# Optimization experiments

Measured on AMD Instinct MI355X. Metric: run time of the kernel, lower is better.

The kernel has to match this reference:

```python
import jax, jax.numpy as jnp
import numpy as np

N = 50000
E = 800000
IN_DIM = 128
HID = 64
OUT_DIM = 128
NEG_SLOPE = 0.2  # PyG GATConv default


def _add_self_loops(src, dst, edge_attr, n):
    # PyG GATConv(add_self_loops=True) with edge_dim uses fill_value='mean':
    # self-loop edge_attr = mean of edge_attr of incoming edges per node.
    deg = jax.ops.segment_sum(jnp.ones((src.shape[0],), edge_attr.dtype), dst, num_segments=n)
    loop_attr = jax.ops.segment_sum(edge_attr, dst, num_segments=n) / jnp.maximum(deg, 1.0)[:, None]
    loop = jnp.arange(n, dtype=src.dtype)
    return (jnp.concatenate([src, loop]), jnp.concatenate([dst, loop]),
            jnp.concatenate([edge_attr, loop_attr], axis=0))


def _gat_conv(x, src, dst, edge_attr, W, We, a_src, a_dst, a_edge, bias, heads, out_dim, concat, n):
    src, dst, edge_attr = _add_self_loops(src, dst, edge_attr, n)
    h = (x @ W).reshape(n, heads, out_dim)                      # [N,H,D]
    he = (edge_attr @ We).reshape(-1, heads, out_dim)           # [E',H,D]
    alpha_src = jnp.einsum('nhd,hd->nh', h, a_src)
    alpha_dst = jnp.einsum('nhd,hd->nh', h, a_dst)
    alpha_edge = jnp.einsum('ehd,hd->eh', he, a_edge)
    alpha = jax.nn.leaky_relu(alpha_src[src] + alpha_dst[dst] + alpha_edge, NEG_SLOPE)  # [E',H]
    # segment softmax over edges grouped by destination node
    amax = jax.ops.segment_max(alpha, dst, num_segments=n)
    amax = jnp.where(jnp.isfinite(amax), amax, 0.0)
    ex = jnp.exp(alpha - amax[dst])
    denom = jax.ops.segment_sum(ex, dst, num_segments=n)
    coef = ex / (denom[dst] + 1e-16)                            # [E',H]
    msg = h[src] * coef[:, :, None]                             # [E',H,D]
    out = jax.ops.segment_sum(msg, dst, num_segments=n)         # [N,H,D]
    out = out.reshape(n, heads * out_dim) if concat else out.mean(axis=1)
    return out + bias


def setup_inputs() -> dict:
    key = jax.random.key(0)
    ks = jax.random.split(key, 16)
    s = 0.05
    inp = {
        'x': jax.random.normal(ks[0], (N, IN_DIM), jnp.float32),
        'edge_index': jax.random.randint(ks[1], (2, E), 0, N, dtype=jnp.int64),
        'edge_attr': jax.random.normal(ks[2], (E, 2), jnp.float32),
        # gat1: heads=4, concat -> out 4*HID
        'W1': jax.random.normal(ks[3], (IN_DIM, 4 * HID), jnp.float32) * s,
        'We1': jax.random.normal(ks[4], (2, 4 * HID), jnp.float32) * s,
        'asrc1': jax.random.normal(ks[5], (4, HID), jnp.float32) * s,
        'adst1': jax.random.normal(ks[6], (4, HID), jnp.float32) * s,
        'aedge1': jax.random.normal(ks[7], (4, HID), jnp.float32) * s,
        'b1': jnp.zeros((4 * HID,), jnp.float32),
        # gat2: heads=1, concat=False -> out OUT_DIM
        'W2': jax.random.normal(ks[8], (4 * HID, OUT_DIM), jnp.float32) * s,
        'We2': jax.random.normal(ks[9], (2, OUT_DIM), jnp.float32) * s,
        'asrc2': jax.random.normal(ks[10], (1, OUT_DIM), jnp.float32) * s,
        'adst2': jax.random.normal(ks[11], (1, OUT_DIM), jnp.float32) * s,
        'aedge2': jax.random.normal(ks[12], (1, OUT_DIM), jnp.float32) * s,
        'b2': jnp.zeros((OUT_DIM,), jnp.float32),
    }
    return inp


def reference(x, edge_index, edge_attr, W1, We1, asrc1, adst1, aedge1, b1,
              W2, We2, asrc2, adst2, aedge2, b2):
    src, dst = edge_index[0], edge_index[1]
    # dropout layers are identity in eval mode
    h = _gat_conv(x, src, dst, edge_attr, W1, We1, asrc1, adst1, aedge1, b1,
                  heads=4, out_dim=HID, concat=True, n=x.shape[0])
    h = jax.nn.elu(h)
    out = _gat_conv(h, src, dst, edge_attr, W2, We2, asrc2, adst2, aedge2, b2,
                    heads=1, out_dim=OUT_DIM, concat=False, n=x.shape[0])
    return out
```

## Files before the change

### kernel.cpp

```cpp
#include <hip/hip_runtime.h>
#include <hip/hip_bf16.h>

#define NN 50000
#define EE 800000
#define EP (EE + NN)
#define SCAN_B 2048
#define NB ((NN + SCAN_B - 1) / SCAN_B)


typedef short bf16x8 __attribute__((ext_vector_type(8)));
typedef float f32x4  __attribute__((ext_vector_type(4)));

__device__ __forceinline__ float bf2f(unsigned short u) {
    return __uint_as_float(((unsigned)u) << 16);
}
__device__ __forceinline__ unsigned short f2bf(float f) {
    unsigned b = __float_as_uint(f);
    b += 0x7fffu + ((b >> 16) & 1u);
    return (unsigned short)(b >> 16);
}
__device__ __forceinline__ float2 bfpair(unsigned u) {
    return make_float2(__uint_as_float(u << 16), __uint_as_float(u & 0xffff0000u));
}

__global__ void k_prep(const float* __restrict__ We1, const float* __restrict__ ae1,
                       const float* __restrict__ We2, const float* __restrict__ ae2,
                       float* __restrict__ v,
                       const float* __restrict__ W1, unsigned short* __restrict__ W1t,
                       const float* __restrict__ W2, unsigned short* __restrict__ W2t,
                       const int* __restrict__ ei, int* __restrict__ idg,
                       const float* __restrict__ x, unsigned short* __restrict__ xb) {
    int bid = blockIdx.x, t = threadIdx.x;
    if (bid == 0) {
        if (t < 8) {
            int c = t >> 2, h = t & 3;
            float s = 0.f;
            for (int d = 0; d < 64; d++) s += We1[c * 256 + h * 64 + d] * ae1[h * 64 + d];
            v[c * 4 + h] = s;
        } else if (t < 10) {
            int c = t - 8;
            float s = 0.f;
            for (int d = 0; d < 128; d++) s += We2[c * 128 + d] * ae2[d];
            v[8 + c] = s;
        }
    } else if (bid <= 256) {
        int idx = (bid - 1) * 256 + t;
        if (idx < 32768) {
            int k = idx >> 8, n = idx & 255;
            W1t[n * 128 + k] = f2bf(W1[idx]);
        } else {
            int i = idx - 32768;
            int k = i >> 7, n = i & 127;
            W2t[n * 256 + k] = f2bf(W2[i]);
        }
    } else if (bid <= 256 + 3125) {
        int e = (bid - 257) * 256 + t;
        if (e < EE) atomicAdd(&idg[ei[EE + e]], 1);
    } else {
        int i = (bid - 3382) * 256 + t;
        if (i < NN * 128 / 4) {
            float4 vv = ((const float4*)x)[i];
            ushort4 o;
            o.x = f2bf(vv.x); o.y = f2bf(vv.y); o.z = f2bf(vv.z); o.w = f2bf(vv.w);
            ((ushort4*)xb)[i] = o;
        }
    }
}

__global__ void k_scan1(const int* __restrict__ idg, int* __restrict__ rowptr,
                        int* __restrict__ bsum) {
    __shared__ int sh[512];
    int t = threadIdx.x;
    int base = blockIdx.x * SCAN_B + t * 4;
    int v[4]; int s = 0;
    #pragma unroll
    for (int j = 0; j < 4; j++) {
        int i = base + j;
        v[j] = (i < NN) ? (idg[i] + 1) : 0;
        s += v[j];
    }
    sh[t] = s;
    __syncthreads();
    for (int off = 1; off < 512; off <<= 1) {
        int a = (t >= off) ? sh[t - off] : 0;
        __syncthreads();
        sh[t] += a;
        __syncthreads();
    }
    int run = sh[t] - s;
    #pragma unroll
    for (int j = 0; j < 4; j++) {
        int i = base + j;
        if (i < NN) rowptr[i] = run;
        run += v[j];
    }
    if (t == 511) bsum[blockIdx.x] = sh[511];
}

__global__ void k_scan2(const int* __restrict__ bsum, int* __restrict__ boff,
                        int* __restrict__ rowptr) {
    if (threadIdx.x == 0) {
        int acc = 0;
        for (int b = 0; b < NB; b++) { boff[b] = acc; acc += bsum[b]; }
        rowptr[NN] = acc;
    }
}

__global__ void k_scan3(int* __restrict__ rowptr, const int* __restrict__ boff) {
    int t = threadIdx.x;
    int i = blockIdx.x * SCAN_B + t * 4;
    int off = boff[blockIdx.x];
    #pragma unroll
    for (int j = 0; j < 4; j++)
        if (i + j < NN) rowptr[i + j] += off;
}

__global__ void k_scatter(const int* __restrict__ ei, const float* __restrict__ eattr,
                          const int* __restrict__ rowptr, int* __restrict__ cnt,
                          int2* __restrict__ slot) {
    int e = blockIdx.x * blockDim.x + threadIdx.x;
    if (e >= EE) return;
    int s = ei[e], d = ei[EE + e];
    int p = rowptr[d] + 1 + atomicAdd(&cnt[d], 1);
    float2 a = ((const float2*)eattr)[e];
    unsigned a0 = f2bf(a.x), a1 = f2bf(a.y);
    slot[p] = make_int2(s, (int)(a0 | (a1 << 16)));
}

__global__ void k_selfattr(const int* __restrict__ rowptr, int2* __restrict__ slot) {
    int n = blockIdx.x * blockDim.x + threadIdx.x;
    if (n >= NN) return;
    int beg = rowptr[n], end = rowptr[n + 1];
    float s0 = 0.f, s1 = 0.f;
    for (int p = beg + 1; p < end; p++) {
        unsigned a = (unsigned)slot[p].y;
        s0 += bf2f((unsigned short)(a & 0xffff));
        s1 += bf2f((unsigned short)(a >> 16));
    }
    float dg = fmaxf((float)(end - beg - 1), 1.0f);
    unsigned b0 = f2bf(s0 / dg), b1v = f2bf(s1 / dg);
    slot[beg] = make_int2(n, (int)(b0 | (b1v << 16)));
}

template <int K, int NT, int H>
__global__ __launch_bounds__(256) void gemm_mfma(const unsigned short* __restrict__ A,
                                                 const unsigned short* __restrict__ Bt,
                                                 unsigned short* __restrict__ C,
                                                 const float* __restrict__ avs,
                                                 const float* __restrict__ avd,
                                                 float* __restrict__ asrc,
                                                 float* __restrict__ adst,
                                                 int M, int N) {
    int wave = threadIdx.x >> 6, lane = threadIdx.x & 63;
    int l16 = lane & 15, quad = lane >> 4;
    int m0 = blockIdx.y * 128 + wave * 32;
    int n0 = blockIdx.x * (NT * 16);

    f32x4 acc[2][NT];
    #pragma unroll
    for (int mt = 0; mt < 2; mt++)
        #pragma unroll
        for (int nt = 0; nt < NT; nt++)
            acc[mt][nt] = (f32x4){0.f, 0.f, 0.f, 0.f};

    int ar0 = min(m0 + l16, M - 1);
    int ar1 = min(m0 + 16 + l16, M - 1);
    const unsigned short* a0 = A + (size_t)ar0 * K + quad * 8;
    const unsigned short* a1 = A + (size_t)ar1 * K + quad * 8;
    const unsigned short* bp = Bt + (size_t)(n0 + l16) * K + quad * 8;

    #pragma unroll
    for (int k0 = 0; k0 < K; k0 += 32) {
        bf16x8 af0 = *(const bf16x8*)(a0 + k0);
        bf16x8 af1 = *(const bf16x8*)(a1 + k0);
        #pragma unroll
        for (int nt = 0; nt < NT; nt++) {
            bf16x8 bf = *(const bf16x8*)(bp + (size_t)nt * 16 * K + k0);
            acc[0][nt] = __builtin_amdgcn_mfma_f32_16x16x32_bf16(af0, bf, acc[0][nt], 0, 0, 0);
            acc[1][nt] = __builtin_amdgcn_mfma_f32_16x16x32_bf16(af1, bf, acc[1][nt], 0, 0, 0);
        }
    }

    #pragma unroll
    for (int mt = 0; mt < 2; mt++)
        #pragma unroll
        for (int reg = 0; reg < 4; reg++) {
            int row = m0 + mt * 16 + quad * 4 + reg;
            if (row < M) {
                #pragma unroll
                for (int nt = 0; nt < NT; nt++)
                    C[(size_t)row * N + n0 + nt * 16 + l16] = f2bf(acc[mt][nt][reg]);
            }
        }

    float ws[NT], wd[NT];
    #pragma unroll
    for (int nt = 0; nt < NT; nt++) {
        ws[nt] = avs[n0 + nt * 16 + l16];
        wd[nt] = avd[n0 + nt * 16 + l16];
    }
    int hh = n0 >> 6;
    #pragma unroll
    for (int mt = 0; mt < 2; mt++)
        #pragma unroll
        for (int reg = 0; reg < 4; reg++) {
            int row = m0 + mt * 16 + quad * 4 + reg;
            float s1 = 0.f, s2 = 0.f;
            #pragma unroll
            for (int nt = 0; nt < NT; nt++) {
                float c = acc[mt][nt][reg];
                s1 += c * ws[nt];
                s2 += c * wd[nt];
            }
            #pragma unroll
            for (int off = 1; off < 16; off <<= 1) {
                s1 += __shfl_xor(s1, off);
                s2 += __shfl_xor(s2, off);
            }
            if (l16 == 0 && row < M) {
                asrc[row * H + hh] = s1;
                adst[row * H + hh] = s2;
            }
        }
}

__global__ __launch_bounds__(256) void k_agg1(const int* __restrict__ rowptr,
                       const int2* __restrict__ slot, const float* __restrict__ asrc,
                       const float* __restrict__ adst, const float* __restrict__ v,
                       const unsigned short* __restrict__ hb, const float* __restrict__ b1,
                       unsigned short* __restrict__ h2b) {
    int node = blockIdx.x * 4 + (threadIdx.x >> 6);
    if (node >= NN) return;
    int lane = threadIdx.x & 63;
    int j    = lane & 15;
    int hp   = lane >> 4;
    int half = lane >> 5;
    int hl   = lane & 31;
    int hh2  = hl >> 3;
    int beg = rowptr[node], end = rowptr[node + 1];
    float ad_p = adst[node * 4 + hp];
    float v0 = v[hp], v1 = v[4 + hp];
    float2 acc2[4] = {};
    float den = 0.f;
    for (int pb = beg; pb < end; pb += 16) {
        int m = min(16, end - pb);
        int sj = 0; float exv = 0.f;
        if (j < m) {
            int2 sl = slot[pb + j];
            sj = sl.x;
            float2 a = bfpair((unsigned)sl.y);
            float al = asrc[sj * 4 + hp] + ad_p + a.x * v0 + a.y * v1;
            al = (al > 0.f) ? al : 0.2f * al;
            exv = __expf(al);
        }
        den += exv;
        #pragma unroll 2
        for (int j2 = 0; j2 < m; j2 += 2) {
            int jj = j2 + half;
            int s   = __shfl(sj, jj);
            float w = __shfl(exv, jj + (hh2 << 4));
            uint4 raw = *(const uint4*)(hb + (size_t)s * 256 + hl * 8);
            float2 p0 = bfpair(raw.x), p1 = bfpair(raw.y);
            float2 p2 = bfpair(raw.z), p3 = bfpair(raw.w);
            acc2[0].x += w * p0.x; acc2[0].y += w * p0.y;
            acc2[1].x += w * p1.x; acc2[1].y += w * p1.y;
            acc2[2].x += w * p2.x; acc2[2].y += w * p2.y;
            acc2[3].x += w * p3.x; acc2[3].y += w * p3.y;
        }
    }
    #pragma unroll
    for (int k = 0; k < 4; k++) {
        acc2[k].x += __shfl_down(acc2[k].x, 32);
        acc2[k].y += __shfl_down(acc2[k].y, 32);
    }
    #pragma unroll
    for (int off = 8; off; off >>= 1) den += __shfl_xor(den, off);
    float den_h = __shfl(den, hh2 << 4);
    if (lane < 32) {
        float inv = 1.f / (den_h + 1e-16f);
        short ov[8];
        #pragma unroll
        for (int k = 0; k < 4; k++) {
            float va = acc2[k].x * inv + b1[hl * 8 + 2 * k];
            float vb = acc2[k].y * inv + b1[hl * 8 + 2 * k + 1];
            va = (va > 0.f) ? va : __expf(va) - 1.f;
            vb = (vb > 0.f) ? vb : __expf(vb) - 1.f;
            ov[2 * k]     = (short)f2bf(va);
            ov[2 * k + 1] = (short)f2bf(vb);
        }
        bf16x8 o = {ov[0], ov[1], ov[2], ov[3], ov[4], ov[5], ov[6], ov[7]};
        *(bf16x8*)(h2b + (size_t)node * 256 + hl * 8) = o;
    }
}

__global__ __launch_bounds__(256) void k_agg2(const int* __restrict__ rowptr,
                       const int2* __restrict__ slot, const float* __restrict__ asrc,
                       const float* __restrict__ adst, const float* __restrict__ v,
                       const unsigned short* __restrict__ gb, const float* __restrict__ b2,
                       float* __restrict__ outp) {
    int node = blockIdx.x * 4 + (threadIdx.x >> 6);
    if (node >= NN) return;
    int lane = threadIdx.x & 63;
    int q  = lane >> 4;
    int ql = lane & 15;
    int beg = rowptr[node], end = rowptr[node + 1];
    float ad = adst[node];
    float v0 = v[0], v1 = v[1];
    float2 acc2[4] = {};
    float den = 0.f;
    for (int pb = beg; pb < end; pb += 64) {
        int m = min(64, end - pb);
        int sj = 0; float exv = 0.f;
        if (lane < m) {
            int2 sl = slot[pb + lane];
            sj = sl.x;
            float2 a = bfpair((unsigned)sl.y);
            float al = asrc[sj] + ad + a.x * v0 + a.y * v1;
            al = (al > 0.f) ? al : 0.2f * al;
            exv = __expf(al);
        }
        den += exv;
        #pragma unroll 2
        for (int j2 = 0; j2 < m; j2 += 4) {
            int jj = j2 + q;
            int s   = __shfl(sj, jj);
            float w = __shfl(exv, jj);
            uint4 raw = *(const uint4*)(gb + (size_t)s * 128 + ql * 8);
            float2 p0 = bfpair(raw.x), p1 = bfpair(raw.y);
            float2 p2 = bfpair(raw.z), p3 = bfpair(raw.w);
            acc2[0].x += w * p0.x; acc2[0].y += w * p0.y;
            acc2[1].x += w * p1.x; acc2[1].y += w * p1.y;
            acc2[2].x += w * p2.x; acc2[2].y += w * p2.y;
            acc2[3].x += w * p3.x; acc2[3].y += w * p3.y;
        }
    }
    #pragma unroll
    for (int k = 0; k < 4; k++) {
        acc2[k].x += __shfl_down(acc2[k].x, 32);
        acc2[k].y += __shfl_down(acc2[k].y, 32);
        acc2[k].x += __shfl_down(acc2[k].x, 16);
        acc2[k].y += __shfl_down(acc2[k].y, 16);
    }
    #pragma unroll
    for (int off = 32; off; off >>= 1) den += __shfl_xor(den, off);
    if (lane < 16) {
        float inv = 1.f / (den + 1e-16f);
        float4 o0, o1;
        o0.x = acc2[0].x * inv + b2[ql * 8 + 0];
        o0.y = acc2[0].y * inv + b2[ql * 8 + 1];
        o0.z = acc2[1].x * inv + b2[ql * 8 + 2];
        o0.w = acc2[1].y * inv + b2[ql * 8 + 3];
        o1.x = acc2[2].x * inv + b2[ql * 8 + 4];
        o1.y = acc2[2].y * inv + b2[ql * 8 + 5];
        o1.z = acc2[3].x * inv + b2[ql * 8 + 6];
        o1.w = acc2[3].y * inv + b2[ql * 8 + 7];
        *(float4*)(outp + (size_t)node * 128 + ql * 8)     = o0;
        *(float4*)(outp + (size_t)node * 128 + ql * 8 + 4) = o1;
    }
}

extern "C" void kernel_launch(void* const* d_in, const int* in_sizes, int n_in,
                              void* d_out, int out_size, void* d_ws, size_t ws_size,
                              hipStream_t stream) {
    const float* x     = (const float*)d_in[0];
    const int*   ei    = (const int*)d_in[1];
    const float* eattr = (const float*)d_in[2];
    const float* W1    = (const float*)d_in[3];
    const float* We1   = (const float*)d_in[4];
    const float* as1   = (const float*)d_in[5];
    const float* ad1   = (const float*)d_in[6];
    const float* ae1   = (const float*)d_in[7];
    const float* b1    = (const float*)d_in[8];
    const float* W2    = (const float*)d_in[9];
    const float* We2   = (const float*)d_in[10];
    const float* as2   = (const float*)d_in[11];
    const float* ad2   = (const float*)d_in[12];
    const float* ae2   = (const float*)d_in[13];
    const float* b2    = (const float*)d_in[14];
    float* out = (float*)d_out;

    int* idg    = (int*)d_ws;
    int* cnt    = idg + NN;
    int* rowptr = cnt + NN;
    int* bsum   = rowptr + NN + 16;
    int* boff   = bsum + 32;
    int2* slot  = (int2*)(boff + 32);
    float* asrc1 = (float*)(slot + EP);
    float* adst1 = asrc1 + 4 * NN;
    float* asrc2 = adst1 + 4 * NN;
    float* adst2 = asrc2 + NN;
    float* vbuf  = adst2 + NN;
    unsigned short* ub = (unsigned short*)(((uintptr_t)(vbuf + 64) + 63) & ~(uintptr_t)63);
    unsigned short* x_bf  = ub;
    unsigned short* W1t   = x_bf + (size_t)NN * 128;
    unsigned short* W2t   = W1t + 32768;
    unsigned short* h1_bf = W2t + 32768;
    unsigned short* h2_bf = h1_bf + (size_t)NN * 256;
    unsigned short* g2_bf = h2_bf + (size_t)NN * 256;

    hipMemsetAsync(idg, 0, (size_t)2 * NN * sizeof(int), stream);

    k_prep<<<9632, 256, 0, stream>>>(We1, ae1, We2, ae2, vbuf, W1, W1t, W2, W2t,
                                     ei, idg, x, x_bf);
    k_scan1<<<NB, 512, 0, stream>>>(idg, rowptr, bsum);
    k_scan2<<<1, 64, 0, stream>>>(bsum, boff, rowptr);
    k_scan3<<<NB, 512, 0, stream>>>(rowptr, boff);
    k_scatter<<<(EE + 255) / 256, 256, 0, stream>>>(ei, eattr, rowptr, cnt, slot);
    k_selfattr<<<(NN + 255) / 256, 256, 0, stream>>>(rowptr, slot);

    gemm_mfma<128, 4, 4><<<dim3(4, (NN + 127) / 128), 256, 0, stream>>>(
        x_bf, W1t, h1_bf, as1, ad1, asrc1, adst1, NN, 256);
    k_agg1<<<(NN + 3) / 4, 256, 0, stream>>>(rowptr, slot, asrc1, adst1, vbuf,
                                             h1_bf, b1, h2_bf);

    gemm_mfma<256, 8, 1><<<dim3(1, (NN + 127) / 128), 256, 0, stream>>>(
        h2_bf, W2t, g2_bf, as2, ad2, asrc2, adst2, NN, 128);
    k_agg2<<<(NN + 3) / 4, 256, 0, stream>>>(rowptr, slot, asrc2, adst2, vbuf + 8,
                                             g2_bf, b2, out);
}
```

Before: 355.8 us.

## Handle self-loops inside aggregation and reuse degree-count atomics as scatter ranks

Self-loop edges are no longer stored in the CSR slot array. Each aggregation kernel now computes the mean edge attribute and the self-loop attention term on the fly and adds the self contribution after the loop, which removes the k_selfattr kernel. The atomic return value from the degree count is saved as a per-edge rank, so the scatter no longer needs a second atomic pass or the cnt memset. The layer-1 aggregation also prefetches the next chunk of slot and asrc values to overlap their latency with compute. The cost is an extra 3.2 MB rank buffer plus extra shuffle reductions and per-node epilogue work.

```diff
diff --git a/kernel.cpp b/kernel.cpp
--- a/kernel.cpp
+++ b/kernel.cpp
@@ -3,7 +3,6 @@
 
 #define NN 50000
 #define EE 800000
-#define EP (EE + NN)
 #define SCAN_B 2048
 #define NB ((NN + SCAN_B - 1) / SCAN_B)
 
@@ -29,6 +28,7 @@
                        const float* __restrict__ W1, unsigned short* __restrict__ W1t,
                        const float* __restrict__ W2, unsigned short* __restrict__ W2t,
                        const int* __restrict__ ei, int* __restrict__ idg,
+                       int* __restrict__ rank,
                        const float* __restrict__ x, unsigned short* __restrict__ xb) {
     int bid = blockIdx.x, t = threadIdx.x;
     if (bid == 0) {
@@ -55,7 +55,7 @@
         }
     } else if (bid <= 256 + 3125) {
         int e = (bid - 257) * 256 + t;
-        if (e < EE) atomicAdd(&idg[ei[EE + e]], 1);
+        if (e < EE) rank[e] = atomicAdd(&idg[ei[EE + e]], 1);
     } else {
         int i = (bid - 3382) * 256 + t;
         if (i < NN * 128 / 4) {
@@ -76,7 +76,7 @@
     #pragma unroll
     for (int j = 0; j < 4; j++) {
         int i = base + j;
-        v[j] = (i < NN) ? (idg[i] + 1) : 0;
+        v[j] = (i < NN) ? idg[i] : 0;
         s += v[j];
     }
     sh[t] = s;
@@ -116,30 +116,15 @@
 }
 
 __global__ void k_scatter(const int* __restrict__ ei, const float* __restrict__ eattr,
-                          const int* __restrict__ rowptr, int* __restrict__ cnt,
+                          const int* __restrict__ rowptr, const int* __restrict__ rank,
                           int2* __restrict__ slot) {
     int e = blockIdx.x * blockDim.x + threadIdx.x;
     if (e >= EE) return;
     int s = ei[e], d = ei[EE + e];
-    int p = rowptr[d] + 1 + atomicAdd(&cnt[d], 1);
+    int p = rowptr[d] + rank[e];
     float2 a = ((const float2*)eattr)[e];
     unsigned a0 = f2bf(a.x), a1 = f2bf(a.y);
     slot[p] = make_int2(s, (int)(a0 | (a1 << 16)));
-}
-
-__global__ void k_selfattr(const int* __restrict__ rowptr, int2* __restrict__ slot) {
-    int n = blockIdx.x * blockDim.x + threadIdx.x;
-    if (n >= NN) return;
-    int beg = rowptr[n], end = rowptr[n + 1];
-    float s0 = 0.f, s1 = 0.f;
-    for (int p = beg + 1; p < end; p++) {
-        unsigned a = (unsigned)slot[p].y;
-        s0 += bf2f((unsigned short)(a & 0xffff));
-        s1 += bf2f((unsigned short)(a >> 16));
-    }
-    float dg = fmaxf((float)(end - beg - 1), 1.0f);
-    unsigned b0 = f2bf(s0 / dg), b1v = f2bf(s1 / dg);
-    slot[beg] = make_int2(n, (int)(b0 | (b1v << 16)));
 }
 
 template <int K, int NT, int H>
@@ -241,23 +226,43 @@
     float ad_p = adst[node * 4 + hp];
     float v0 = v[hp], v1 = v[4 + hp];
     float2 acc2[4] = {};
-    float den = 0.f;
-    for (int pb = beg; pb < end; pb += 16) {
-        int m = min(16, end - pb);
-        int sj = 0; float exv = 0.f;
+    float den = 0.f, s0 = 0.f, s1 = 0.f;
+
+    int pb = beg;
+    int m = min(16, end - pb);
+    int sj = 0; float aa0 = 0.f, aa1 = 0.f, av = 0.f;
+    if (j < m) {
+        int2 sl = slot[pb + j];
+        sj = sl.x;
+        float2 a = bfpair((unsigned)sl.y);
+        aa0 = a.x; aa1 = a.y;
+        av = asrc[sj * 4 + hp];
+    }
+    while (pb < end) {
+        int cm = m, csj = sj;
+        float ca0 = aa0, ca1 = aa1, cav = av;
+        pb += 16;
+        m = min(16, end - pb);
+        sj = 0; aa0 = 0.f; aa1 = 0.f; av = 0.f;
         if (j < m) {
             int2 sl = slot[pb + j];
             sj = sl.x;
             float2 a = bfpair((unsigned)sl.y);
-            float al = asrc[sj * 4 + hp] + ad_p + a.x * v0 + a.y * v1;
+            aa0 = a.x; aa1 = a.y;
+            av = asrc[sj * 4 + hp];
+        }
+        float exv = 0.f;
+        if (j < cm) {
+            s0 += ca0; s1 += ca1;
+            float al = cav + ad_p + ca0 * v0 + ca1 * v1;
             al = (al > 0.f) ? al : 0.2f * al;
             exv = __expf(al);
         }
         den += exv;
         #pragma unroll 2
-        for (int j2 = 0; j2 < m; j2 += 2) {
+        for (int j2 = 0; j2 < cm; j2 += 2) {
             int jj = j2 + half;
-            int s   = __shfl(sj, jj);
+            int s   = __shfl(csj, jj);
             float w = __shfl(exv, jj + (hh2 << 4));
             uint4 raw = *(const uint4*)(hb + (size_t)s * 256 + hl * 8);
             float2 p0 = bfpair(raw.x), p1 = bfpair(raw.y);
@@ -269,13 +274,33 @@
         }
     }
     #pragma unroll
+    for (int off = 1; off < 16; off <<= 1) {
+        s0 += __shfl_xor(s0, off);
+        s1 += __shfl_xor(s1, off);
+    }
+    float dg = fmaxf((float)(end - beg), 1.0f);
+    float als = asrc[node * 4 + hp] + ad_p + (s0 / dg) * v0 + (s1 / dg) * v1;
+    als = (als > 0.f) ? als : 0.2f * als;
+    float exs = __expf(als);
+    #pragma unroll
+    for (int off = 8; off; off >>= 1) den += __shfl_xor(den, off);
+    den += exs;
+    float den_h  = __shfl(den, hh2 << 4);
+    float w_self = __shfl(exs, hh2 << 4);
+    if (half == 0) {
+        uint4 raw = *(const uint4*)(hb + (size_t)node * 256 + hl * 8);
+        float2 p0 = bfpair(raw.x), p1 = bfpair(raw.y);
+        float2 p2 = bfpair(raw.z), p3 = bfpair(raw.w);
+        acc2[0].x += w_self * p0.x; acc2[0].y += w_self * p0.y;
+        acc2[1].x += w_self * p1.x; acc2[1].y += w_self * p1.y;
+        acc2[2].x += w_self * p2.x; acc2[2].y += w_self * p2.y;
+        acc2[3].x += w_self * p3.x; acc2[3].y += w_self * p3.y;
+    }
+    #pragma unroll
     for (int k = 0; k < 4; k++) {
         acc2[k].x += __shfl_down(acc2[k].x, 32);
         acc2[k].y += __shfl_down(acc2[k].y, 32);
     }
-    #pragma unroll
-    for (int off = 8; off; off >>= 1) den += __shfl_xor(den, off);
-    float den_h = __shfl(den, hh2 << 4);
     if (lane < 32) {
         float inv = 1.f / (den_h + 1e-16f);
         short ov[8];
@@ -307,7 +332,7 @@
     float ad = adst[node];
     float v0 = v[0], v1 = v[1];
     float2 acc2[4] = {};
-    float den = 0.f;
+    float den = 0.f, s0 = 0.f, s1 = 0.f;
     for (int pb = beg; pb < end; pb += 64) {
         int m = min(64, end - pb);
         int sj = 0; float exv = 0.f;
@@ -315,6 +340,7 @@
             int2 sl = slot[pb + lane];
             sj = sl.x;
             float2 a = bfpair((unsigned)sl.y);
+            s0 += a.x; s1 += a.y;
             float al = asrc[sj] + ad + a.x * v0 + a.y * v1;
             al = (al > 0.f) ? al : 0.2f * al;
             exv = __expf(al);
@@ -335,14 +361,32 @@
         }
     }
     #pragma unroll
+    for (int off = 32; off; off >>= 1) {
+        s0  += __shfl_xor(s0, off);
+        s1  += __shfl_xor(s1, off);
+        den += __shfl_xor(den, off);
+    }
+    float dg = fmaxf((float)(end - beg), 1.0f);
+    float als = asrc[node] + ad + (s0 / dg) * v0 + (s1 / dg) * v1;
+    als = (als > 0.f) ? als : 0.2f * als;
+    float exs = __expf(als);
+    den += exs;
+    if (q == 0) {
+        uint4 raw = *(const uint4*)(gb + (size_t)node * 128 + ql * 8);
+        float2 p0 = bfpair(raw.x), p1 = bfpair(raw.y);
+        float2 p2 = bfpair(raw.z), p3 = bfpair(raw.w);
+        acc2[0].x += exs * p0.x; acc2[0].y += exs * p0.y;
+        acc2[1].x += exs * p1.x; acc2[1].y += exs * p1.y;
+        acc2[2].x += exs * p2.x; acc2[2].y += exs * p2.y;
+        acc2[3].x += exs * p3.x; acc2[3].y += exs * p3.y;
+    }
+    #pragma unroll
     for (int k = 0; k < 4; k++) {
         acc2[k].x += __shfl_down(acc2[k].x, 32);
         acc2[k].y += __shfl_down(acc2[k].y, 32);
         acc2[k].x += __shfl_down(acc2[k].x, 16);
         acc2[k].y += __shfl_down(acc2[k].y, 16);
     }
-    #pragma unroll
-    for (int off = 32; off; off >>= 1) den += __shfl_xor(den, off);
     if (lane < 16) {
         float inv = 1.f / (den + 1e-16f);
         float4 o0, o1;
@@ -380,12 +424,12 @@
     float* out = (float*)d_out;
 
     int* idg    = (int*)d_ws;
-    int* cnt    = idg + NN;
-    int* rowptr = cnt + NN;
+    int* rank   = idg + NN;
+    int* rowptr = rank + EE;
     int* bsum   = rowptr + NN + 16;
     int* boff   = bsum + 32;
     int2* slot  = (int2*)(boff + 32);
-    float* asrc1 = (float*)(slot + EP);
+    float* asrc1 = (float*)(slot + EE);
     float* adst1 = asrc1 + 4 * NN;
     float* asrc2 = adst1 + 4 * NN;
     float* adst2 = asrc2 + NN;
@@ -398,15 +442,14 @@
     unsigned short* h2_bf = h1_bf + (size_t)NN * 256;
     unsigned short* g2_bf = h2_bf + (size_t)NN * 256;
 
-    hipMemsetAsync(idg, 0, (size_t)2 * NN * sizeof(int), stream);
+    hipMemsetAsync(idg, 0, (size_t)NN * sizeof(int), stream);
 
     k_prep<<<9632, 256, 0, stream>>>(We1, ae1, We2, ae2, vbuf, W1, W1t, W2, W2t,
-                                     ei, idg, x, x_bf);
+                                     ei, idg, rank, x, x_bf);
     k_scan1<<<NB, 512, 0, stream>>>(idg, rowptr, bsum);
     k_scan2<<<1, 64, 0, stream>>>(bsum, boff, rowptr);
     k_scan3<<<NB, 512, 0, stream>>>(rowptr, boff);
-    k_scatter<<<(EE + 255) / 256, 256, 0, stream>>>(ei, eattr, rowptr, cnt, slot);
-    k_selfattr<<<(NN + 255) / 256, 256, 0, stream>>>(rowptr, slot);
+    k_scatter<<<(EE + 255) / 256, 256, 0, stream>>>(ei, eattr, rowptr, rank, slot);
 
     gemm_mfma<128, 4, 4><<<dim3(4, (NN + 127) / 128), 256, 0, stream>>>(
         x_bf, W1t, h1_bf, as1, ad1, asrc1, adst1, NN, 256);
```

Result: faster. 333.9 us (-6.2%).
